# Optimization experiments

Hardware: AMD Instinct MI355X
Metric: run time of the kernel (lower is better)

The kernel has to match this reference:

```python
import jax, jax.numpy as jnp
import numpy as np

N, D, I, O = 4096, 64, 512, 512  # samples, node_nums (bases), input_size, output_size


def setup_inputs() -> dict:
    key = jax.random.key(0)
    k1, k2, k3, k4 = jax.random.split(key, 4)
    # xavier_uniform bounds
    w_bound = float(np.sqrt(6.0 / (I + O)))
    b_bound = float(np.sqrt(6.0 / (D + O)))
    return {
        "x": jax.random.normal(k1, (N, I), dtype=jnp.float32),
        "var_vector": jax.random.uniform(k2, (N, D), dtype=jnp.float32),
        "W_1": jax.random.uniform(k3, (D, I, O), dtype=jnp.float32, minval=-w_bound, maxval=w_bound),
        "b_1": jax.random.uniform(k4, (D, O), dtype=jnp.float32, minval=-b_bound, maxval=b_bound),
    }


def reference(x, var_vector, W_1, b_1):
    # Math identical to: einsum('nd,dio->nio') then bmm(x[:,None,:], W)[:,0,:] + b.
    # Reordered contraction: contract x against each basis first (never forms n,i,o).
    y = jnp.einsum('ni,dio->ndo', x, W_1)        # [n, d, o]
    out = jnp.einsum('nd,ndo->no', var_vector, y)  # [n, o]
    b = jnp.einsum('nd,do->no', var_vector, b_1)   # [n, o]
    return out + b
```

## Files before the change

kernel.cpp:

```cpp
#include <hip/hip_runtime.h>
#include <hip/hip_bf16.h>
#include <stdint.h>
#include <stddef.h>

#define N_ 4096
#define D_ 64
#define I_ 512
#define O_ 512

#define BM 256
#define BN 128
#define BK 64
#define SPLITS 4
#define DPG 16
#define PAIRS (DPG / 2)
#define KSTEPS (I_ / BK)
#define NSTEP (PAIRS * KSTEPS)

typedef float  floatx4 __attribute__((ext_vector_type(4)));
typedef short  shortx8 __attribute__((ext_vector_type(8)));

__device__ __forceinline__ void gload_lds16(const void* g, void* l) {
  __builtin_amdgcn_global_load_lds(
      (const __attribute__((address_space(1))) void*)g,
      (__attribute__((address_space(3))) void*)l, 16, 0, 0);
}

__device__ __forceinline__ unsigned short f2bf(float f) {
  union { float f; unsigned int u; } c; c.f = f;
  unsigned int u = c.u;
  return (unsigned short)((u + 0x7fffu + ((u >> 16) & 1u)) >> 16);
}

__device__ __forceinline__ void mfma_bf16(floatx4& c, shortx8 a, shortx8 b) {
  asm("v_mfma_f32_16x16x32_bf16 %0, %1, %2, %0" : "+v"(c) : "v"(a), "v"(b));
}

__global__ void k_cvt_x(const float* __restrict__ x, unsigned short* __restrict__ xb) {
  int idx = (blockIdx.x * blockDim.x + threadIdx.x) * 8;
  floatx4 a = *(const floatx4*)(x + idx);
  floatx4 b = *(const floatx4*)(x + idx + 4);
  shortx8 o;
  o[0] = (short)f2bf(a[0]); o[1] = (short)f2bf(a[1]);
  o[2] = (short)f2bf(a[2]); o[3] = (short)f2bf(a[3]);
  o[4] = (short)f2bf(b[0]); o[5] = (short)f2bf(b[1]);
  o[6] = (short)f2bf(b[2]); o[7] = (short)f2bf(b[3]);
  *(shortx8*)(xb + idx) = o;
}

__global__ void k_cvt_w(const float* __restrict__ w, unsigned short* __restrict__ wt) {
  __shared__ unsigned short T[64][72];
  int bid = blockIdx.x;
  int d  = bid >> 6;
  int it = (bid >> 3) & 7;
  int ot = bid & 7;
  int i0 = it * 64, o0 = ot * 64;
  int t = threadIdx.x;
  const float* wp = w + ((size_t)d * I_ + i0) * O_ + o0;
  #pragma unroll
  for (int j = 0; j < 16; ++j) {
    int idx = j * 256 + t;
    int r = idx >> 6, c = idx & 63;
    T[r][c] = f2bf(wp[(size_t)r * O_ + c]);
  }
  __syncthreads();
  unsigned short* op = wt + ((size_t)d * O_ + o0) * I_ + i0;
  #pragma unroll
  for (int j = 0; j < 16; ++j) {
    int idx = j * 256 + t;
    int r = idx >> 6, c = idx & 63;
    op[(size_t)r * I_ + c] = T[c][r];
  }
}

__global__ void k_bias(const float* __restrict__ var, const float* __restrict__ b1,
                       float* __restrict__ out) {
  __shared__ float vs[16][64];
  int n0 = blockIdx.x * 16;
  int t = threadIdx.x;
  #pragma unroll
  for (int j = 0; j < 4; ++j) {
    int idx = j * 256 + t;
    vs[idx >> 6][idx & 63] = var[(size_t)n0 * D_ + idx];
  }
  __syncthreads();
  float a0[16], a1[16];
  #pragma unroll
  for (int r = 0; r < 16; ++r) { a0[r] = 0.f; a1[r] = 0.f; }
  for (int d = 0; d < D_; ++d) {
    float b0 = b1[(size_t)d * O_ + t];
    float bb = b1[(size_t)d * O_ + 256 + t];
    #pragma unroll
    for (int r = 0; r < 16; ++r) { a0[r] += vs[r][d] * b0; a1[r] += vs[r][d] * bb; }
  }
  #pragma unroll
  for (int r = 0; r < 16; ++r) {
    out[(size_t)(n0 + r) * O_ + t]       = a0[r];
    out[(size_t)(n0 + r) * O_ + 256 + t] = a1[r];
  }
}

__global__ __launch_bounds__(512, 2) void k_gemm(
    const unsigned short* __restrict__ xb, const unsigned short* __restrict__ wt,
    const float* __restrict__ var, float* __restrict__ out) {
  __shared__ alignas(16) unsigned short lA[2][BM * BK];
  __shared__ alignas(16) unsigned short lB[2][2][BN * BK];
  __shared__ alignas(16) float lV[DPG * BM];

  const int tid = threadIdx.x;
  const int bid = blockIdx.x;
  const int g  = bid & 15;
  const int mt = bid >> 4;
  const int ot = g >> 2, split = g & 3;
  const int brow = mt * BM, bcol = ot * BN, d0 = split * DPG;

  const int lane = tid & 63, wid = tid >> 6;
  const int wr = wid >> 1, wc = wid & 1;
  const int l15 = lane & 15, l4 = lane >> 4;

  #pragma unroll
  for (int j = 0; j < (DPG * BM) / 512; ++j) {
    int idx = j * 512 + tid;
    int dd = idx >> 8, row = idx & (BM - 1);
    lV[idx] = var[(size_t)(brow + row) * D_ + d0 + dd];
  }

  auto stage = [&](int s, int buf) {
    const int p  = s >> 3;
    const int kk = s & 7;
    const int da = d0 + 2 * p;
    const char* xsrc = (const char*)xb + ((size_t)brow * I_ + (size_t)kk * BK) * 2;
    const char* w0 = (const char*)wt + (((size_t)da * O_ + bcol) * I_ + (size_t)kk * BK) * 2;
    const char* w1 = (const char*)wt + (((size_t)(da + 1) * O_ + bcol) * I_ + (size_t)kk * BK) * 2;
    char* la  = (char*)&lA[buf][0];
    char* lb0 = (char*)&lB[buf][0][0];
    char* lb1 = (char*)&lB[buf][1][0];
    #pragma unroll
    for (int c = 0; c < 4; ++c) {
      int pb = (c * 512 + tid) << 4;
      int row = pb >> 7;
      int colG = (pb & 127) ^ ((row & 7) << 4);
      gload_lds16(xsrc + (size_t)row * (I_ * 2) + colG, la + pb);
    }
    #pragma unroll
    for (int c = 0; c < 2; ++c) {
      int pb = (c * 512 + tid) << 4;
      int row = pb >> 7;
      int colG = (pb & 127) ^ ((row & 7) << 4);
      gload_lds16(w0 + (size_t)row * (I_ * 2) + colG, lb0 + pb);
      gload_lds16(w1 + (size_t)row * (I_ * 2) + colG, lb1 + pb);
    }
  };

  stage(0, 0);

  const floatx4 vzero = {0.f, 0.f, 0.f, 0.f};
  floatx4 master[4][4];
  #pragma unroll
  for (int m = 0; m < 4; ++m)
    #pragma unroll
    for (int n = 0; n < 4; ++n) master[m][n] = vzero;

  __syncthreads();

  for (int p = 0; p < PAIRS; ++p) {
    floatx4 acc0[4][4], acc1[4][4];
    #pragma unroll
    for (int m = 0; m < 4; ++m)
      #pragma unroll
      for (int n = 0; n < 4; ++n) { acc0[m][n] = vzero; acc1[m][n] = vzero; }

    for (int kk = 0; kk < KSTEPS; ++kk) {
      const int s = p * KSTEPS + kk;
      const int buf = s & 1;
      if (s + 1 < NSTEP) {
        stage(s + 1, (s + 1) & 1);
        asm volatile("s_waitcnt vmcnt(8)" ::: "memory");
      } else {
        asm volatile("s_waitcnt vmcnt(0)" ::: "memory");
      }
      const char* laB  = (const char*)&lA[buf][0];
      const char* lb0B = (const char*)&lB[buf][0][0];
      const char* lb1B = (const char*)&lB[buf][1][0];
      __builtin_amdgcn_s_setprio(1);
      #pragma unroll
      for (int ks = 0; ks < 2; ++ks) {
        const int cb = ks * 64 + l4 * 16;
        shortx8 av[4];
        #pragma unroll
        for (int m = 0; m < 4; ++m) {
          int row = wr * 64 + m * 16 + l15;
          av[m] = *(const shortx8*)(laB + row * 128 + (cb ^ ((row & 7) << 4)));
        }
        shortx8 bv[4];
        #pragma unroll
        for (int n = 0; n < 4; ++n) {
          int row = wc * 64 + n * 16 + l15;
          bv[n] = *(const shortx8*)(lb0B + row * 128 + (cb ^ ((row & 7) << 4)));
        }
        #pragma unroll
        for (int m = 0; m < 4; ++m)
          #pragma unroll
          for (int n = 0; n < 4; ++n) mfma_bf16(acc0[m][n], av[m], bv[n]);
        #pragma unroll
        for (int n = 0; n < 4; ++n) {
          int row = wc * 64 + n * 16 + l15;
          bv[n] = *(const shortx8*)(lb1B + row * 128 + (cb ^ ((row & 7) << 4)));
        }
        #pragma unroll
        for (int m = 0; m < 4; ++m)
          #pragma unroll
          for (int n = 0; n < 4; ++n) mfma_bf16(acc1[m][n], av[m], bv[n]);
      }
      __builtin_amdgcn_s_setprio(0);
      __builtin_amdgcn_s_barrier();
    }

    #pragma unroll
    for (int m = 0; m < 4; ++m) {
      int rbase = wr * 64 + m * 16 + l4 * 4;
      floatx4 v0 = *(const floatx4*)&lV[(2 * p) * BM + rbase];
      floatx4 v1 = *(const floatx4*)&lV[(2 * p + 1) * BM + rbase];
      #pragma unroll
      for (int n = 0; n < 4; ++n)
        #pragma unroll
        for (int r = 0; r < 4; ++r)
          master[m][n][r] += v0[r] * acc0[m][n][r] + v1[r] * acc1[m][n][r];
    }
  }

  #pragma unroll
  for (int m = 0; m < 4; ++m) {
    int row0 = brow + wr * 64 + m * 16 + l4 * 4;
    #pragma unroll
    for (int n = 0; n < 4; ++n) {
      int col = bcol + wc * 64 + n * 16 + l15;
      #pragma unroll
      for (int r = 0; r < 4; ++r)
        atomicAdd(out + (size_t)(row0 + r) * O_ + col, master[m][n][r]);
    }
  }
}

__global__ void k_naive(const float* __restrict__ x, const float* __restrict__ var,
                        const float* __restrict__ w, const float* __restrict__ b1,
                        float* __restrict__ out) {
  int n = blockIdx.x;
  int o = blockIdx.y * 128 + threadIdx.x;
  const float* xp = x + (size_t)n * I_;
  float acc = 0.f;
  for (int d = 0; d < D_; ++d) {
    const float* wp = w + (size_t)d * I_ * O_ + o;
    float y = 0.f;
    for (int i = 0; i < I_; ++i) y += xp[i] * wp[(size_t)i * O_];
    acc += var[(size_t)n * D_ + o % 1 * 0 + d] * (y + b1[(size_t)d * O_ + o]);
  }
  out[(size_t)n * O_ + o] = acc;
}

extern "C" void kernel_launch(void* const* d_in, const int* in_sizes, int n_in,
                              void* d_out, int out_size, void* d_ws, size_t ws_size,
                              hipStream_t stream) {
  const float* x   = (const float*)d_in[0];
  const float* var = (const float*)d_in[1];
  const float* W   = (const float*)d_in[2];
  const float* b1  = (const float*)d_in[3];
  float* out = (float*)d_out;

  const size_t wt_bytes = (size_t)D_ * I_ * O_ * 2;
  const size_t xb_bytes = (size_t)N_ * I_ * 2;
  if (ws_size >= wt_bytes + xb_bytes) {
    unsigned short* wt = (unsigned short*)d_ws;
    unsigned short* xb = (unsigned short*)((char*)d_ws + wt_bytes);
    k_cvt_x<<<dim3((N_ * I_) / (256 * 8)), dim3(256), 0, stream>>>(x, xb);
    k_cvt_w<<<dim3(D_ * 64), dim3(256), 0, stream>>>(W, wt);
    k_bias<<<dim3(N_ / 16), dim3(256), 0, stream>>>(var, b1, out);
    k_gemm<<<dim3((N_ / BM) * (O_ / BN) * SPLITS), dim3(512), 0, stream>>>(xb, wt, var, out);
  } else {
    k_naive<<<dim3(N_, O_ / 128), dim3(128), 0, stream>>>(x, var, W, b1, out);
  }
}
```

Baseline: 190.0 us.

## Interleave global prefetch with MFMA phases and drop occupancy launch bound

Splits each k-step into four barrier-separated MFMA phases. The next stage's A and B global-to-LDS loads are issued between LDS reads and MFMA clusters, so memory traffic interleaves with compute the way ping-pong scheduling does. It also removes the min-blocks-per-CU hint from launch bounds, letting the compiler use more registers. The risks are extra barriers, a full vmcnt(0) wait at the end of every step, and possibly lower occupancy.

```diff
diff --git a/kernel.cpp b/kernel.cpp
--- a/kernel.cpp
+++ b/kernel.cpp
@@ -100,7 +100,7 @@
   }
 }
 
-__global__ __launch_bounds__(512, 2) void k_gemm(
+__global__ __launch_bounds__(512) void k_gemm(
     const unsigned short* __restrict__ xb, const unsigned short* __restrict__ wt,
     const float* __restrict__ var, float* __restrict__ out) {
   __shared__ alignas(16) unsigned short lA[2][BM * BK];
@@ -125,34 +125,34 @@
     lV[idx] = var[(size_t)(brow + row) * D_ + d0 + dd];
   }
 
-  auto stage = [&](int s, int buf) {
-    const int p  = s >> 3;
+  const char* xbB = (const char*)xb;
+  const char* wtB = (const char*)wt;
+
+  auto stage_A2 = [&](int s, int buf, int c0) {
     const int kk = s & 7;
-    const int da = d0 + 2 * p;
-    const char* xsrc = (const char*)xb + ((size_t)brow * I_ + (size_t)kk * BK) * 2;
-    const char* w0 = (const char*)wt + (((size_t)da * O_ + bcol) * I_ + (size_t)kk * BK) * 2;
-    const char* w1 = (const char*)wt + (((size_t)(da + 1) * O_ + bcol) * I_ + (size_t)kk * BK) * 2;
-    char* la  = (char*)&lA[buf][0];
-    char* lb0 = (char*)&lB[buf][0][0];
-    char* lb1 = (char*)&lB[buf][1][0];
-    #pragma unroll
-    for (int c = 0; c < 4; ++c) {
+    const char* xsrc = xbB + ((size_t)brow * I_ + (size_t)kk * BK) * 2;
+    char* la = (char*)&lA[buf][0];
+    #pragma unroll
+    for (int c = c0; c < c0 + 2; ++c) {
       int pb = (c * 512 + tid) << 4;
       int row = pb >> 7;
       int colG = (pb & 127) ^ ((row & 7) << 4);
       gload_lds16(xsrc + (size_t)row * (I_ * 2) + colG, la + pb);
     }
-    #pragma unroll
-    for (int c = 0; c < 2; ++c) {
-      int pb = (c * 512 + tid) << 4;
-      int row = pb >> 7;
-      int colG = (pb & 127) ^ ((row & 7) << 4);
-      gload_lds16(w0 + (size_t)row * (I_ * 2) + colG, lb0 + pb);
-      gload_lds16(w1 + (size_t)row * (I_ * 2) + colG, lb1 + pb);
-    }
   };
-
-  stage(0, 0);
+  auto stage_B2 = [&](int s, int buf, int c) {
+    const int p = s >> 3, kk = s & 7;
+    const int da = d0 + 2 * p;
+    const char* w0 = wtB + (((size_t)da * O_ + bcol) * I_ + (size_t)kk * BK) * 2;
+    int pb = (c * 512 + tid) << 4;
+    int row = pb >> 7;
+    int colG = (pb & 127) ^ ((row & 7) << 4);
+    gload_lds16(w0 + (size_t)row * (I_ * 2) + colG, (char*)&lB[buf][0][0] + pb);
+    gload_lds16(w0 + (size_t)O_ * I_ * 2 + (size_t)row * (I_ * 2) + colG,
+                (char*)&lB[buf][1][0] + pb);
+  };
+
+  stage_A2(0, 0, 0); stage_A2(0, 0, 2); stage_B2(0, 0, 0); stage_B2(0, 0, 1);
 
   const floatx4 vzero = {0.f, 0.f, 0.f, 0.f};
   floatx4 master[4][4];
@@ -161,6 +161,7 @@
     #pragma unroll
     for (int n = 0; n < 4; ++n) master[m][n] = vzero;
 
+  asm volatile("s_waitcnt vmcnt(0)" ::: "memory");
   __syncthreads();
 
   for (int p = 0; p < PAIRS; ++p) {
@@ -173,46 +174,87 @@
     for (int kk = 0; kk < KSTEPS; ++kk) {
       const int s = p * KSTEPS + kk;
       const int buf = s & 1;
-      if (s + 1 < NSTEP) {
-        stage(s + 1, (s + 1) & 1);
-        asm volatile("s_waitcnt vmcnt(8)" ::: "memory");
-      } else {
-        asm volatile("s_waitcnt vmcnt(0)" ::: "memory");
-      }
+      const bool pre = (s + 1 < NSTEP);
       const char* laB  = (const char*)&lA[buf][0];
       const char* lb0B = (const char*)&lB[buf][0][0];
       const char* lb1B = (const char*)&lB[buf][1][0];
+      shortx8 av[4], bv[4];
+
+      #pragma unroll
+      for (int m = 0; m < 4; ++m) {
+        int row = wr * 64 + m * 16 + l15;
+        av[m] = *(const shortx8*)(laB + row * 128 + ((l4 * 16) ^ ((row & 7) << 4)));
+      }
+      #pragma unroll
+      for (int n = 0; n < 4; ++n) {
+        int row = wc * 64 + n * 16 + l15;
+        bv[n] = *(const shortx8*)(lb0B + row * 128 + ((l4 * 16) ^ ((row & 7) << 4)));
+      }
+      if (pre) { stage_A2(s + 1, buf ^ 1, 0); stage_A2(s + 1, buf ^ 1, 2); }
+      __builtin_amdgcn_s_barrier();
+      asm volatile("s_waitcnt lgkmcnt(0)" ::: "memory");
+      __builtin_amdgcn_sched_barrier(0);
       __builtin_amdgcn_s_setprio(1);
       #pragma unroll
-      for (int ks = 0; ks < 2; ++ks) {
-        const int cb = ks * 64 + l4 * 16;
-        shortx8 av[4];
-        #pragma unroll
-        for (int m = 0; m < 4; ++m) {
-          int row = wr * 64 + m * 16 + l15;
-          av[m] = *(const shortx8*)(laB + row * 128 + (cb ^ ((row & 7) << 4)));
-        }
-        shortx8 bv[4];
-        #pragma unroll
-        for (int n = 0; n < 4; ++n) {
-          int row = wc * 64 + n * 16 + l15;
-          bv[n] = *(const shortx8*)(lb0B + row * 128 + (cb ^ ((row & 7) << 4)));
-        }
-        #pragma unroll
-        for (int m = 0; m < 4; ++m)
-          #pragma unroll
-          for (int n = 0; n < 4; ++n) mfma_bf16(acc0[m][n], av[m], bv[n]);
-        #pragma unroll
-        for (int n = 0; n < 4; ++n) {
-          int row = wc * 64 + n * 16 + l15;
-          bv[n] = *(const shortx8*)(lb1B + row * 128 + (cb ^ ((row & 7) << 4)));
-        }
-        #pragma unroll
-        for (int m = 0; m < 4; ++m)
-          #pragma unroll
-          for (int n = 0; n < 4; ++n) mfma_bf16(acc1[m][n], av[m], bv[n]);
-      }
+      for (int m = 0; m < 4; ++m)
+        #pragma unroll
+        for (int n = 0; n < 4; ++n) mfma_bf16(acc0[m][n], av[m], bv[n]);
       __builtin_amdgcn_s_setprio(0);
+      __builtin_amdgcn_s_barrier();
+
+      #pragma unroll
+      for (int n = 0; n < 4; ++n) {
+        int row = wc * 64 + n * 16 + l15;
+        bv[n] = *(const shortx8*)(lb1B + row * 128 + ((l4 * 16) ^ ((row & 7) << 4)));
+      }
+      if (pre) { stage_B2(s + 1, buf ^ 1, 0); stage_B2(s + 1, buf ^ 1, 1); }
+      __builtin_amdgcn_s_barrier();
+      asm volatile("s_waitcnt lgkmcnt(0)" ::: "memory");
+      __builtin_amdgcn_sched_barrier(0);
+      __builtin_amdgcn_s_setprio(1);
+      #pragma unroll
+      for (int m = 0; m < 4; ++m)
+        #pragma unroll
+        for (int n = 0; n < 4; ++n) mfma_bf16(acc1[m][n], av[m], bv[n]);
+      __builtin_amdgcn_s_setprio(0);
+      __builtin_amdgcn_s_barrier();
+
+      #pragma unroll
+      for (int m = 0; m < 4; ++m) {
+        int row = wr * 64 + m * 16 + l15;
+        av[m] = *(const shortx8*)(laB + row * 128 + ((64 + l4 * 16) ^ ((row & 7) << 4)));
+      }
+      #pragma unroll
+      for (int n = 0; n < 4; ++n) {
+        int row = wc * 64 + n * 16 + l15;
+        bv[n] = *(const shortx8*)(lb0B + row * 128 + ((64 + l4 * 16) ^ ((row & 7) << 4)));
+      }
+      __builtin_amdgcn_s_barrier();
+      asm volatile("s_waitcnt lgkmcnt(0)" ::: "memory");
+      __builtin_amdgcn_sched_barrier(0);
+      __builtin_amdgcn_s_setprio(1);
+      #pragma unroll
+      for (int m = 0; m < 4; ++m)
+        #pragma unroll
+        for (int n = 0; n < 4; ++n) mfma_bf16(acc0[m][n], av[m], bv[n]);
+      __builtin_amdgcn_s_setprio(0);
+      __builtin_amdgcn_s_barrier();
+
+      #pragma unroll
+      for (int n = 0; n < 4; ++n) {
+        int row = wc * 64 + n * 16 + l15;
+        bv[n] = *(const shortx8*)(lb1B + row * 128 + ((64 + l4 * 16) ^ ((row & 7) << 4)));
+      }
+      __builtin_amdgcn_s_barrier();
+      asm volatile("s_waitcnt lgkmcnt(0)" ::: "memory");
+      __builtin_amdgcn_sched_barrier(0);
+      __builtin_amdgcn_s_setprio(1);
+      #pragma unroll
+      for (int m = 0; m < 4; ++m)
+        #pragma unroll
+        for (int n = 0; n < 4; ++n) mfma_bf16(acc1[m][n], av[m], bv[n]);
+      __builtin_amdgcn_s_setprio(0);
+      asm volatile("s_waitcnt vmcnt(0)" ::: "memory");
       __builtin_amdgcn_s_barrier();
     }
 
@@ -253,7 +295,7 @@
     const float* wp = w + (size_t)d * I_ * O_ + o;
     float y = 0.f;
     for (int i = 0; i < I_; ++i) y += xp[i] * wp[(size_t)i * O_];
-    acc += var[(size_t)n * D_ + o % 1 * 0 + d] * (y + b1[(size_t)d * O_ + o]);
+    acc += var[(size_t)n * D_ + d] * (y + b1[(size_t)d * O_ + o]);
   }
   out[(size_t)n * O_ + o] = acc;
 }
```

Measured after the change: 178.5 us. 1.06x faster.

## Restructure GEMM mainloop into 4-slot LDS ring with split A/B staging

Applied to the files above, without the earlier changes.

Replaces the double-buffered BK=64 staging with a 4-slot ring of 32-wide K chunks, prefetching two steps ahead. A and B loads are issued separately and interleaved with the two MFMA phases, with finer barriers and vmcnt waits. LDS fragment offsets are precomputed per thread in a remapped swizzled layout. The aim is to overlap global-to-LDS traffic with MFMA work and cut stalls. In exchange it adds barriers per step, and dropping the 2-blocks-per-CU launch bound may change occupancy.

```diff
diff --git a/kernel.cpp b/kernel.cpp
--- a/kernel.cpp
+++ b/kernel.cpp
@@ -10,12 +10,13 @@
 
 #define BM 256
 #define BN 128
-#define BK 64
 #define SPLITS 4
 #define DPG 16
 #define PAIRS (DPG / 2)
-#define KSTEPS (I_ / BK)
-#define NSTEP (PAIRS * KSTEPS)
+#define KXS 16
+#define NS (PAIRS * KXS)
+#define SLOTA (128 * 128)
+#define SLOTB (64 * 128)
 
 typedef float  floatx4 __attribute__((ext_vector_type(4)));
 typedef short  shortx8 __attribute__((ext_vector_type(8)));
@@ -100,11 +101,11 @@
   }
 }
 
-__global__ __launch_bounds__(512, 2) void k_gemm(
+__global__ __launch_bounds__(512) void k_gemm(
     const unsigned short* __restrict__ xb, const unsigned short* __restrict__ wt,
     const float* __restrict__ var, float* __restrict__ out) {
-  __shared__ alignas(16) unsigned short lA[2][BM * BK];
-  __shared__ alignas(16) unsigned short lB[2][2][BN * BK];
+  __shared__ alignas(16) char lA[4][SLOTA];
+  __shared__ alignas(16) char lB[4][2][SLOTB];
   __shared__ alignas(16) float lV[DPG * BM];
 
   const int tid = threadIdx.x;
@@ -125,34 +126,61 @@
     lV[idx] = var[(size_t)(brow + row) * D_ + d0 + dd];
   }
 
-  auto stage = [&](int s, int buf) {
-    const int p  = s >> 3;
-    const int kk = s & 7;
-    const int da = d0 + 2 * p;
-    const char* xsrc = (const char*)xb + ((size_t)brow * I_ + (size_t)kk * BK) * 2;
-    const char* w0 = (const char*)wt + (((size_t)da * O_ + bcol) * I_ + (size_t)kk * BK) * 2;
-    const char* w1 = (const char*)wt + (((size_t)(da + 1) * O_ + bcol) * I_ + (size_t)kk * BK) * 2;
-    char* la  = (char*)&lA[buf][0];
-    char* lb0 = (char*)&lB[buf][0][0];
-    char* lb1 = (char*)&lB[buf][1][0];
-    #pragma unroll
-    for (int c = 0; c < 4; ++c) {
-      int pb = (c * 512 + tid) << 4;
-      int row = pb >> 7;
-      int colG = (pb & 127) ^ ((row & 7) << 4);
-      gload_lds16(xsrc + (size_t)row * (I_ * 2) + colG, la + pb);
-    }
-    #pragma unroll
-    for (int c = 0; c < 2; ++c) {
-      int pb = (c * 512 + tid) << 4;
-      int row = pb >> 7;
-      int colG = (pb & 127) ^ ((row & 7) << 4);
-      gload_lds16(w0 + (size_t)row * (I_ * 2) + colG, lb0 + pb);
-      gload_lds16(w1 + (size_t)row * (I_ * 2) + colG, lb1 + pb);
-    }
+  const char* xbB = (const char*)xb;
+  const char* wtB = (const char*)wt;
+
+  int pbA[2]; size_t gbA[2];
+  #pragma unroll
+  for (int c = 0; c < 2; ++c) {
+    int pb = (c * 512 + tid) << 4;
+    int rl = pb >> 7;
+    int colG = (pb & 127) ^ ((rl & 7) << 4);
+    int r_src = rl + ((colG >> 6) << 7);
+    int k_src = (colG & 63) >> 1;
+    pbA[c] = pb;
+    gbA[c] = ((size_t)(brow + r_src) * I_ + k_src) * 2;
+  }
+  int pbB; size_t gbB;
+  {
+    int pb = tid << 4;
+    int rl = pb >> 7;
+    int colG = (pb & 127) ^ ((rl & 7) << 4);
+    int r_src = rl + ((colG >> 6) << 6);
+    int k_src = (colG & 63) >> 1;
+    pbB = pb;
+    gbB = ((size_t)(bcol + r_src) * I_ + k_src) * 2;
+  }
+
+  int avOff[4], bvOff[4];
+  #pragma unroll
+  for (int m = 0; m < 4; ++m) {
+    int r = wr * 64 + m * 16 + l15;
+    int rl = r & 127;
+    avOff[m] = rl * 128 + ((((r >> 7) << 6) + l4 * 16) ^ ((rl & 7) << 4));
+  }
+  #pragma unroll
+  for (int n = 0; n < 4; ++n) {
+    int r = wc * 64 + n * 16 + l15;
+    int rl = r & 63;
+    bvOff[n] = rl * 128 + (((wc << 6) + l4 * 16) ^ ((rl & 7) << 4));
+  }
+
+  auto stage_A = [&](int s) {
+    const int kx = s & 15;
+    char* la = (char*)&lA[s & 3][0];
+    #pragma unroll
+    for (int c = 0; c < 2; ++c)
+      gload_lds16(xbB + gbA[c] + (size_t)kx * 64, la + pbA[c]);
   };
-
-  stage(0, 0);
+  auto stage_B = [&](int s) {
+    const int d = d0 + 2 * (s >> 4);
+    const int kx = s & 15;
+    const char* src = wtB + (size_t)d * (I_ * O_ * 2) + gbB + (size_t)kx * 64;
+    gload_lds16(src, (char*)&lB[s & 3][0][0] + pbB);
+    gload_lds16(src + (size_t)(I_ * O_ * 2), (char*)&lB[s & 3][1][0] + pbB);
+  };
+
+  stage_A(0); stage_B(0); stage_A(1); stage_B(1);
 
   const floatx4 vzero = {0.f, 0.f, 0.f, 0.f};
   floatx4 master[4][4];
@@ -161,7 +189,9 @@
     #pragma unroll
     for (int n = 0; n < 4; ++n) master[m][n] = vzero;
 
-  __syncthreads();
+  asm volatile("s_waitcnt vmcnt(4) lgkmcnt(0)" ::: "memory");
+  __builtin_amdgcn_sched_barrier(0);
+  __builtin_amdgcn_s_barrier();
 
   for (int p = 0; p < PAIRS; ++p) {
     floatx4 acc0[4][4], acc1[4][4];
@@ -170,49 +200,44 @@
       #pragma unroll
       for (int n = 0; n < 4; ++n) { acc0[m][n] = vzero; acc1[m][n] = vzero; }
 
-    for (int kk = 0; kk < KSTEPS; ++kk) {
-      const int s = p * KSTEPS + kk;
-      const int buf = s & 1;
-      if (s + 1 < NSTEP) {
-        stage(s + 1, (s + 1) & 1);
-        asm volatile("s_waitcnt vmcnt(8)" ::: "memory");
-      } else {
-        asm volatile("s_waitcnt vmcnt(0)" ::: "memory");
-      }
-      const char* laB  = (const char*)&lA[buf][0];
-      const char* lb0B = (const char*)&lB[buf][0][0];
-      const char* lb1B = (const char*)&lB[buf][1][0];
+    #pragma unroll 1
+    for (int kx = 0; kx < KXS; ++kx) {
+      const int s = p * KXS + kx;
+      const char* aS  = (const char*)&lA[s & 3][0];
+      const char* bS0 = (const char*)&lB[s & 3][0][0];
+      const char* bS1 = (const char*)&lB[s & 3][1][0];
+      shortx8 av[4], bv[4];
+
+      #pragma unroll
+      for (int m = 0; m < 4; ++m) av[m] = *(const shortx8*)(aS + avOff[m]);
+      #pragma unroll
+      for (int n = 0; n < 4; ++n) bv[n] = *(const shortx8*)(bS0 + bvOff[n]);
+      if (s + 2 < NS) stage_A(s + 2);
+      __builtin_amdgcn_s_barrier();
+      asm volatile("s_waitcnt lgkmcnt(0)" ::: "memory");
+      __builtin_amdgcn_sched_barrier(0);
       __builtin_amdgcn_s_setprio(1);
       #pragma unroll
-      for (int ks = 0; ks < 2; ++ks) {
-        const int cb = ks * 64 + l4 * 16;
-        shortx8 av[4];
+      for (int m = 0; m < 4; ++m)
         #pragma unroll
-        for (int m = 0; m < 4; ++m) {
-          int row = wr * 64 + m * 16 + l15;
-          av[m] = *(const shortx8*)(laB + row * 128 + (cb ^ ((row & 7) << 4)));
-        }
-        shortx8 bv[4];
+        for (int n = 0; n < 4; ++n) mfma_bf16(acc0[m][n], av[m], bv[n]);
+      __builtin_amdgcn_s_setprio(0);
+      __builtin_amdgcn_s_barrier();
+
+      #pragma unroll
+      for (int n = 0; n < 4; ++n) bv[n] = *(const shortx8*)(bS1 + bvOff[n]);
+      if (s + 2 < NS) stage_B(s + 2);
+      __builtin_amdgcn_s_barrier();
+      asm volatile("s_waitcnt lgkmcnt(0)" ::: "memory");
+      __builtin_amdgcn_sched_barrier(0);
+      __builtin_amdgcn_s_setprio(1);
+      #pragma unroll
+      for (int m = 0; m < 4; ++m)
         #pragma unroll
-        for (int n = 0; n < 4; ++n) {
-          int row = wc * 64 + n * 16 + l15;
-          bv[n] = *(const shortx8*)(lb0B + row * 128 + (cb ^ ((row & 7) << 4)));
-        }
-        #pragma unroll
-        for (int m = 0; m < 4; ++m)
-          #pragma unroll
-          for (int n = 0; n < 4; ++n) mfma_bf16(acc0[m][n], av[m], bv[n]);
-        #pragma unroll
-        for (int n = 0; n < 4; ++n) {
-          int row = wc * 64 + n * 16 + l15;
-          bv[n] = *(const shortx8*)(lb1B + row * 128 + (cb ^ ((row & 7) << 4)));
-        }
-        #pragma unroll
-        for (int m = 0; m < 4; ++m)
-          #pragma unroll
-          for (int n = 0; n < 4; ++n) mfma_bf16(acc1[m][n], av[m], bv[n]);
-      }
+        for (int n = 0; n < 4; ++n) mfma_bf16(acc1[m][n], av[m], bv[n]);
       __builtin_amdgcn_s_setprio(0);
+      if (s + 2 < NS) { asm volatile("s_waitcnt vmcnt(4)" ::: "memory"); }
+      else            { asm volatile("s_waitcnt vmcnt(0)" ::: "memory"); }
       __builtin_amdgcn_s_barrier();
     }
 
@@ -253,7 +278,7 @@
     const float* wp = w + (size_t)d * I_ * O_ + o;
     float y = 0.f;
     for (int i = 0; i < I_; ++i) y += xp[i] * wp[(size_t)i * O_];
-    acc += var[(size_t)n * D_ + o % 1 * 0 + d] * (y + b1[(size_t)d * O_ + o]);
+    acc += var[(size_t)n * D_ + d] * (y + b1[(size_t)d * O_ + o]);
   }
   out[(size_t)n * O_ + o] = acc;
 }
```

Measured after the change: 186.6 us. No clear change (-1.8%).
